# Kernel tuning notes

Hardware: AMD Instinct MI355X
Metric: run time of the kernel (lower is better)

Reference implementation:

```python
import jax, jax.numpy as jnp
import numpy as np
from jax import lax

B, C, H, W = 32, 64, 56, 56
G = 4            # num_heads*2 with num_heads=2
SMK, K = 5, 7
C2 = C // 2
HEAD_DIM = C // G
SCALE = HEAD_DIM ** -0.5


def _bias_idx(k, h, w):
    # static replica of ContMix.generate_idx + apply_rpb index construction
    rpb_size = 2 * k - 1
    idx_h = np.arange(k)
    idx_w = np.arange(k)
    idx_k = (idx_h[:, None] * rpb_size + idx_w).reshape(-1)
    rep_h = np.ones(k, np.int64); rep_h[k // 2] = h - (k - 1)
    rep_w = np.ones(k, np.int64); rep_w[k // 2] = w - (k - 1)
    bias_hw = np.repeat(idx_h, rep_h)[:, None] * rpb_size + np.repeat(idx_w, rep_w)  # (h, w)
    bias_idx = (bias_hw[..., None] + idx_k).reshape(-1, k * k)[::-1]  # torch.flip dim 0
    return jnp.asarray(bias_idx.copy())

IDX1 = _bias_idx(SMK, H, W)
IDX2 = _bias_idx(K, H, W)


def setup_inputs() -> dict:
    key = jax.random.key(0)
    ks = jax.random.split(key, 18)
    r = lambda i, sh: jax.random.normal(ks[i], sh, jnp.float32)
    return dict(
        x=r(0, (B, C, H, W)),
        lepe_w=r(1, (C, 1, K, K)) * 0.1,
        lepe_b=r(2, (C,)) * 0.1,
        lepe_bn_s=1.0 + 0.1 * r(3, (C,)),
        lepe_bn_b=0.1 * r(4, (C,)),
        wq_w=r(5, (C2, C2)) * (C2 ** -0.5),
        wq_bn_s=1.0 + 0.1 * r(6, (C2,)),
        wq_bn_b=0.1 * r(7, (C2,)),
        wk_w=r(8, (C2, C2)) * (C2 ** -0.5),
        wk_bn_s=1.0 + 0.1 * r(9, (C2,)),
        wk_bn_b=0.1 * r(10, (C2,)),
        wp_w=r(11, (SMK * SMK + K * K, 49)) * (49 ** -0.5),
        wp_b=0.1 * r(12, (SMK * SMK + K * K,)),
        rpb1=0.02 * r(13, (G, 2 * SMK - 1, 2 * SMK - 1)),
        rpb2=0.02 * r(14, (G, 2 * K - 1, 2 * K - 1)),
        dy_w=r(15, (C, C)) * (C ** -0.5),
        dy_bn_s=1.0 + 0.1 * r(16, (C,)),
        dy_bn_b=0.1 * r(17, (C,)),
    )


def _per_ch(t):
    return t[None, :, None, None]


def _contmix(x, lepe_w, lepe_b, lepe_bn_s, lepe_bn_b, wq_w, wq_bn_s, wq_bn_b,
             wk_w, wk_bn_s, wk_bn_b, wp_w, wp_b, rpb1, rpb2, dy_w, dy_bn_s, dy_bn_b):
    # lepe: deploy-mode DilatedReparamBlock = depthwise 7x7 conv (+bias), then eval BN
    lepe = lax.conv_general_dilated(x, lepe_w, (1, 1), [(K // 2, K // 2)] * 2,
                                    feature_group_count=C)
    lepe = (lepe + _per_ch(lepe_b)) * _per_ch(lepe_bn_s) + _per_ch(lepe_bn_b)

    q, kf = jnp.split(x, 2, axis=1)                         # (B, C2, H, W) each
    q = jnp.einsum('oi,bihw->bohw', wq_w, q)                # weight_query 1x1 conv
    q = (q * _per_ch(wq_bn_s) + _per_ch(wq_bn_b)) * SCALE
    # weight_key: AdaptiveAvgPool2d(7) -> 1x1 conv -> BN (H,W divisible by 7)
    kp = kf.reshape(B, C2, 7, H // 7, 7, W // 7).mean(axis=(3, 5))
    kp = jnp.einsum('oi,bihw->bohw', wk_w, kp)
    kp = kp * _per_ch(wk_bn_s) + _per_ch(wk_bn_b)

    qg = q.reshape(B, G, C2 // G, H * W)                    # b g c n
    kg = kp.reshape(B, G, C2 // G, 49)                      # b g c l
    w = jnp.einsum('bgcn,bgcl->bgnl', qg, kg)               # (B, G, HW, 49)
    # weight_proj: 1x1 conv over the 49 pooled-context channels
    w = jnp.einsum('ml,bgnl->bgnm', wp_w, w) + wp_b         # (B, G, HW, 74)
    w = w.reshape(B, G, H, W, SMK * SMK + K * K)

    attn1 = w[..., :SMK * SMK]
    attn2 = w[..., SMK * SMK:]
    attn1 = attn1 + rpb1.reshape(G, -1)[:, IDX1].reshape(1, G, H, W, SMK * SMK)
    attn2 = attn2 + rpb2.reshape(G, -1)[:, IDX2].reshape(1, G, H, W, K * K)
    attn1 = jax.nn.softmax(attn1, axis=-1)
    attn2 = jax.nn.softmax(attn2, axis=-1)

    c = C // (2 * G)                                        # value head dim = 8
    v = x.reshape(B, 2, G, c, H, W)                         # 'b (m g c) h w'

    def dyn_mix(attn, val, k):
        # unfold + einsum: content-adaptive depthwise mixing
        p = lax.conv_general_dilated_patches(
            val.reshape(B, G * c, H, W), (k, k), (1, 1), [(k // 2, k // 2)] * 2,
            dimension_numbers=('NCHW', 'OIHW', 'NCHW'))
        p = p.reshape(B, G, c, k * k, H, W)                 # channel-major patch layout
        return jnp.einsum('bgckhw,bghwk->bgchw', p, attn)

    x1 = dyn_mix(attn1, v[:, 0], SMK)
    x2 = dyn_mix(attn2, v[:, 1], K)
    out = jnp.concatenate([x1, x2], axis=1).reshape(B, C, H, W)
    out = jnp.einsum('oi,bihw->bohw', dy_w, out)            # dyconv_proj 1x1 + BN
    out = out * _per_ch(dy_bn_s) + _per_ch(dy_bn_b)
    return out + lepe


def reference(x, lepe_w, lepe_b, lepe_bn_s, lepe_bn_b, wq_w, wq_bn_s, wq_bn_b,
              wk_w, wk_bn_s, wk_bn_b, wp_w, wp_b, rpb1, rpb2, dy_w, dy_bn_s, dy_bn_b):
    return _contmix(x, lepe_w, lepe_b, lepe_bn_s, lepe_bn_b, wq_w, wq_bn_s, wq_bn_b,
                    wk_w, wk_bn_s, wk_bn_b, wp_w, wp_b, rpb1, rpb2, dy_w, dy_bn_s, dy_bn_b)
```

## Files before the change

kernel.cpp:

```cpp
#include <hip/hip_runtime.h>

#define BB 32
#define CC 64
#define HH 56
#define WW 56
#define HW 3136
#define TW 64
#define TR 12

__global__ __launch_bounds__(256) void prep_k(const float* __restrict__ x,
                                              const float* __restrict__ wk,
                                              const float* __restrict__ wks,
                                              const float* __restrict__ wkb,
                                              const float* __restrict__ wp_w,
                                              float* __restrict__ WK) {
    __shared__ float p_s[32 * 49];
    __shared__ float kg_s[8 * 49];
    const int b = blockIdx.x >> 2;
    const int g = blockIdx.x & 3;
    const int tid = threadIdx.x;
    for (int idx = tid; idx < 1568; idx += 256) {
        const int i = idx / 49, l = idx % 49;
        const int py = l / 7, px = l % 7;
        const float4* xp4 = reinterpret_cast<const float4*>(
            x + ((long)(b * CC + 32 + i)) * HW + py * 8 * WW + px * 8);
        float4 sA = make_float4(0.f, 0.f, 0.f, 0.f);
        float4 sB = make_float4(0.f, 0.f, 0.f, 0.f);
        #pragma unroll
        for (int y = 0; y < 8; ++y) {
            const float4 a = xp4[y * 14];
            const float4 c = xp4[y * 14 + 1];
            sA.x += a.x; sA.y += a.y; sA.z += a.z; sA.w += a.w;
            sB.x += c.x; sB.y += c.y; sB.z += c.z; sB.w += c.w;
        }
        p_s[idx] = (sA.x + sA.y + sA.z + sA.w + sB.x + sB.y + sB.z + sB.w) * (1.f / 64.f);
    }
    __syncthreads();
    for (int idx = tid; idx < 392; idx += 256) {
        const int o8 = idx / 49, l = idx % 49;
        const int o = g * 8 + o8;
        float acc = 0.f;
        #pragma unroll
        for (int i = 0; i < 32; ++i) acc = fmaf(wk[o * 32 + i], p_s[i * 49 + l], acc);
        kg_s[idx] = acc * wks[o] + wkb[o];
    }
    __syncthreads();
    for (int idx = tid; idx < 640; idx += 256) {
        const int c = idx / 80, slot = idx % 80;
        float acc = 0.f;
        int m = -1;
        if (slot < 28) { if (slot < 25) m = slot; }
        else           { if (slot < 77) m = 25 + (slot - 28); }
        if (m >= 0) {
            const float* kp = kg_s + c * 49;
            #pragma unroll
            for (int l = 0; l < 49; ++l) acc = fmaf(wp_w[m * 49 + l], kp[l], acc);
        }
        const long base = (long)blockIdx.x * 640;
        if (slot < 28) WK[base + c * 28 + slot] = acc;
        else           WK[base + 224 + c * 52 + (slot - 28)] = acc;
    }
}

__global__ __launch_bounds__(256) void attnmix_k(const float* __restrict__ x,
                                                 const float* __restrict__ WK,
                                                 const float* __restrict__ wq_w,
                                                 const float* __restrict__ wq_s,
                                                 const float* __restrict__ wq_bb,
                                                 const float* __restrict__ wp_b,
                                                 const float* __restrict__ rpb1,
                                                 const float* __restrict__ rpb2,
                                                 const float* __restrict__ lw,
                                                 const float* __restrict__ lb,
                                                 const float* __restrict__ ls,
                                                 const float* __restrict__ lbb,
                                                 float* __restrict__ mix,
                                                 float* __restrict__ out) {
    __shared__ float tile[8 * TR * TW];
    __shared__ float WK1_s[8 * 28];
    __shared__ float WK2_s[8 * 52];
    __shared__ float wqT_s[32 * 8];
    __shared__ float wpb1_s[25];
    __shared__ float wpb2_s[49];
    __shared__ float rpb1_s[81];
    __shared__ float rpb2_s[169];
    __shared__ float wqbn_s[16];
    __shared__ float lw_s[16 * 49];
    __shared__ float lbn_s[48];
    const int tid = threadIdx.x;
    const int bg = blockIdx.y;
    const int g = bg & 3, b = bg >> 2;

    {
        const float* wkp = WK + (long)bg * 640;
        for (int i = tid; i < 224; i += 256) WK1_s[i] = wkp[i];
        for (int i = tid; i < 416; i += 256) WK2_s[i] = wkp[224 + i];
    }
    {
        const int i = tid >> 3, c = tid & 7;
        wqT_s[tid] = wq_w[(g * 8 + c) * 32 + i];
    }
    if (tid < 25) wpb1_s[tid] = wp_b[tid];
    if (tid >= 32 && tid < 81) wpb2_s[tid - 32] = wp_b[25 + tid - 32];
    if (tid < 81) rpb1_s[tid] = rpb1[g * 81 + tid];
    if (tid < 169) rpb2_s[tid] = rpb2[g * 169 + tid];
    if (tid >= 192 && tid < 200) wqbn_s[tid - 192] = wq_s[g * 8 + tid - 192];
    if (tid >= 200 && tid < 208) wqbn_s[8 + tid - 200] = wq_bb[g * 8 + tid - 200];
    for (int i = tid; i < 784; i += 256) {
        const int ch = i / 49, k = i % 49;
        const int c = (ch < 8) ? (g * 8 + ch) : (32 + g * 8 + ch - 8);
        lw_s[i] = lw[c * 49 + k];
    }
    if (tid < 16) {
        const int c = (tid < 8) ? (g * 8 + tid) : (32 + g * 8 + tid - 8);
        lbn_s[tid] = lb[c]; lbn_s[16 + tid] = ls[c]; lbn_s[32 + tid] = lbb[c];
    }

    const int N0 = blockIdx.x << 8;
    const int ph0 = N0 / WW;
    const int r0 = ph0 - 3;

    {
        const float* xc = x + ((long)b * CC + g * 8) * HW;
        #pragma unroll
        for (int ch = 0; ch < 8; ++ch)
            for (int k = tid; k < TR * TW; k += 256) {
                const int row = k >> 6, lxx = k & 63;
                const int gy = r0 + row, gx = lxx - 3;
                float v = 0.f;
                if ((unsigned)gy < HH && (unsigned)gx < WW) v = xc[ch * HW + gy * WW + gx];
                tile[ch * (TR * TW) + k] = v;
            }
    }
    __syncthreads();

    const int n = N0 + tid;
    const bool valid = n < HW;
    const int nc = valid ? n : HW - 1;
    const int ph = nc / WW, pw = nc % WW;
    const int yr = HH - 1 - ph, xr = WW - 1 - pw;
    const int lrow = ph - r0;
    const int tb0 = (lrow - 3) * TW + pw;

    const float* xb = x + (long)b * CC * HW + nc;

    float q8[8];
    #pragma unroll
    for (int c = 0; c < 8; ++c) q8[c] = 0.f;
    for (int i = 0; i < 32; ++i) {
        const float xv = xb[i * HW];
        #pragma unroll
        for (int c = 0; c < 8; ++c) q8[c] = fmaf(wqT_s[i * 8 + c], xv, q8[c]);
    }
    #pragma unroll
    for (int c = 0; c < 8; ++c)
        q8[c] = (q8[c] * wqbn_s[c] + wqbn_s[8 + c]) * 0.25f;

    __builtin_amdgcn_sched_barrier(0);

    {
        float w1[25];
        #pragma unroll
        for (int m = 0; m < 25; ++m) w1[m] = wpb1_s[m];
        #pragma unroll
        for (int c = 0; c < 8; ++c) {
            const float qv = q8[c];
            #pragma unroll
            for (int m = 0; m < 25; ++m) w1[m] = fmaf(qv, WK1_s[c * 28 + m], w1[m]);
        }
        const int rh5 = yr < 2 ? yr : (yr > 53 ? yr - 51 : 2);
        const int rw5 = xr < 2 ? xr : (xr > 53 ? xr - 51 : 2);
        #pragma unroll
        for (int i = 0; i < 5; ++i)
            #pragma unroll
            for (int j = 0; j < 5; ++j)
                w1[i * 5 + j] += rpb1_s[(rh5 + i) * 9 + (rw5 + j)];
        float mx = -1e30f;
        #pragma unroll
        for (int m = 0; m < 25; ++m) mx = fmaxf(mx, w1[m]);
        float sm = 0.f;
        #pragma unroll
        for (int m = 0; m < 25; ++m) { w1[m] = __expf(w1[m] - mx); sm += w1[m]; }
        const float r = 1.f / sm;
        #pragma unroll
        for (int m = 0; m < 25; ++m) w1[m] *= r;

        float* m0 = mix + ((long)b * CC + g * 8) * HW + nc;
        float* o0 = out + ((long)b * CC + g * 8) * HW + nc;
        #pragma unroll
        for (int ch = 0; ch < 8; ++ch) {
            const float* t = tile + ch * (TR * TW) + tb0;
            const float* lwc = lw_s + ch * 49;
            float a = 0.f, la = 0.f;
            #pragma unroll
            for (int i = 0; i < 7; ++i)
                #pragma unroll
                for (int j = 0; j < 7; ++j) {
                    const float v = t[i * TW + j];
                    la = fmaf(lwc[i * 7 + j], v, la);
                    if (i >= 1 && i <= 5 && j >= 1 && j <= 5)
                        a = fmaf(w1[(i - 1) * 5 + (j - 1)], v, a);
                }
            if (valid) {
                m0[ch * HW] = a;
                o0[ch * HW] = (la + lbn_s[ch]) * lbn_s[16 + ch] + lbn_s[32 + ch];
            }
        }
    }

    __syncthreads();
    {
        const float* xc = x + ((long)b * CC + 32 + g * 8) * HW;
        #pragma unroll
        for (int ch = 0; ch < 8; ++ch)
            for (int k = tid; k < TR * TW; k += 256) {
                const int row = k >> 6, lxx = k & 63;
                const int gy = r0 + row, gx = lxx - 3;
                float v = 0.f;
                if ((unsigned)gy < HH && (unsigned)gx < WW) v = xc[ch * HW + gy * WW + gx];
                tile[ch * (TR * TW) + k] = v;
            }
    }
    __syncthreads();

    {
        float w2[49];
        #pragma unroll
        for (int m = 0; m < 49; ++m) w2[m] = wpb2_s[m];
        #pragma unroll
        for (int c = 0; c < 8; ++c) {
            const float qv = q8[c];
            #pragma unroll
            for (int m = 0; m < 49; ++m) w2[m] = fmaf(qv, WK2_s[c * 52 + m], w2[m]);
        }
        const int rh7 = yr < 3 ? yr : (yr > 52 ? yr - 49 : 3);
        const int rw7 = xr < 3 ? xr : (xr > 52 ? xr - 49 : 3);
        #pragma unroll
        for (int i = 0; i < 7; ++i)
            #pragma unroll
            for (int j = 0; j < 7; ++j)
                w2[i * 7 + j] += rpb2_s[(rh7 + i) * 13 + (rw7 + j)];
        float mx = -1e30f;
        #pragma unroll
        for (int m = 0; m < 49; ++m) mx = fmaxf(mx, w2[m]);
        float sm = 0.f;
        #pragma unroll
        for (int m = 0; m < 49; ++m) { w2[m] = __expf(w2[m] - mx); sm += w2[m]; }
        const float r = 1.f / sm;
        #pragma unroll
        for (int m = 0; m < 49; ++m) w2[m] *= r;

        float* m1 = mix + ((long)b * CC + 32 + g * 8) * HW + nc;
        float* o1 = out + ((long)b * CC + 32 + g * 8) * HW + nc;
        #pragma unroll
        for (int ch = 0; ch < 8; ++ch) {
            const float* t = tile + ch * (TR * TW) + tb0;
            const float* lwc = lw_s + (8 + ch) * 49;
            float a = 0.f, la = 0.f;
            #pragma unroll
            for (int i = 0; i < 7; ++i)
                #pragma unroll
                for (int j = 0; j < 7; ++j) {
                    const float v = t[i * TW + j];
                    la = fmaf(lwc[i * 7 + j], v, la);
                    a = fmaf(w2[i * 7 + j], v, a);
                }
            if (valid) {
                m1[ch * HW] = a;
                o1[ch * HW] = (la + lbn_s[8 + ch]) * lbn_s[16 + 8 + ch] + lbn_s[32 + 8 + ch];
            }
        }
    }
}

__global__ __launch_bounds__(256) void final_k(const float* __restrict__ mix,
                                               const float* __restrict__ dy_w,
                                               const float* __restrict__ s,
                                               const float* __restrict__ bb,
                                               float* __restrict__ out) {
    __shared__ float w_s[64 * 64];
    const int tid = threadIdx.x;
    const int b = blockIdx.y;
    for (int i = tid; i < 4096; i += 256) w_s[(i & 63) * 64 + (i >> 6)] = dy_w[i];
    __syncthreads();
    const int oo = (tid >> 5) * 8;
    const int p4 = blockIdx.x * 32 + (tid & 31);
    if (p4 >= 784) return;
    const float* mp = mix + (long)b * CC * HW + p4 * 4;
    float4 acc[8];
    #pragma unroll
    for (int o = 0; o < 8; ++o) acc[o] = make_float4(0.f, 0.f, 0.f, 0.f);
    for (int i = 0; i < 64; ++i) {
        const float4 mv = *reinterpret_cast<const float4*>(mp + (long)i * HW);
        const float* wr = w_s + i * 64 + oo;
        #pragma unroll
        for (int o = 0; o < 8; ++o) {
            const float wv = wr[o];
            acc[o].x = fmaf(wv, mv.x, acc[o].x);
            acc[o].y = fmaf(wv, mv.y, acc[o].y);
            acc[o].z = fmaf(wv, mv.z, acc[o].z);
            acc[o].w = fmaf(wv, mv.w, acc[o].w);
        }
    }
    float* op = out + (long)b * CC * HW + p4 * 4;
    #pragma unroll
    for (int o = 0; o < 8; ++o) {
        const float sc = s[oo + o], bc = bb[oo + o];
        float4* dst = reinterpret_cast<float4*>(op + (long)(oo + o) * HW);
        float4 prev = *dst;
        prev.x = fmaf(acc[o].x, sc, bc) + prev.x;
        prev.y = fmaf(acc[o].y, sc, bc) + prev.y;
        prev.z = fmaf(acc[o].z, sc, bc) + prev.z;
        prev.w = fmaf(acc[o].w, sc, bc) + prev.w;
        *dst = prev;
    }
}

extern "C" void kernel_launch(void* const* d_in, const int* in_sizes, int n_in,
                              void* d_out, int out_size, void* d_ws, size_t ws_size,
                              hipStream_t stream) {
    const float* x       = (const float*)d_in[0];
    const float* lepe_w  = (const float*)d_in[1];
    const float* lepe_b  = (const float*)d_in[2];
    const float* lepe_s  = (const float*)d_in[3];
    const float* lepe_bb = (const float*)d_in[4];
    const float* wq_w    = (const float*)d_in[5];
    const float* wq_s    = (const float*)d_in[6];
    const float* wq_bb   = (const float*)d_in[7];
    const float* wk_w    = (const float*)d_in[8];
    const float* wk_s    = (const float*)d_in[9];
    const float* wk_bb   = (const float*)d_in[10];
    const float* wp_w    = (const float*)d_in[11];
    const float* wp_b    = (const float*)d_in[12];
    const float* rpb1    = (const float*)d_in[13];
    const float* rpb2    = (const float*)d_in[14];
    const float* dy_w    = (const float*)d_in[15];
    const float* dy_s    = (const float*)d_in[16];
    const float* dy_bb   = (const float*)d_in[17];
    float* out = (float*)d_out;

    float* ws     = (float*)d_ws;
    float* WK_ws  = ws;
    float* mix_ws = WK_ws + 128 * 640;

    const int nTiles = (HW + 255) / 256;

    prep_k<<<dim3(BB * 4), 256, 0, stream>>>(x, wk_w, wk_s, wk_bb, wp_w, WK_ws);
    attnmix_k<<<dim3(nTiles, BB * 4), 256, 0, stream>>>(x, WK_ws, wq_w, wq_s, wq_bb,
                                                        wp_b, rpb1, rpb2,
                                                        lepe_w, lepe_b, lepe_s, lepe_bb,
                                                        mix_ws, out);
    final_k<<<dim3(25, BB), 256, 0, stream>>>(mix_ws, dy_w, dy_s, dy_bb, out);
}
```

Before: 243.5 us.

## Split pooling kernel, interleave channels in tile, read weights from global

```diff
diff --git a/kernel.cpp b/kernel.cpp
--- a/kernel.cpp
+++ b/kernel.cpp
@@ -7,8 +7,31 @@
 #define HW 3136
 #define TW 64
 #define TR 12
-
-__global__ __launch_bounds__(256) void prep_k(const float* __restrict__ x,
+#define CS 12
+
+__global__ __launch_bounds__(256) void pool_k(const float* __restrict__ x,
+                                              float* __restrict__ pool) {
+    const int idx = blockIdx.x * 256 + threadIdx.x;
+    if (idx >= BB * 32 * 49) return;
+    const int l = idx % 49;
+    const int bi = idx / 49;
+    const int i = bi % 32, b = bi / 32;
+    const int py = l / 7, px = l % 7;
+    const float4* xp4 = reinterpret_cast<const float4*>(
+        x + ((long)(b * CC + 32 + i)) * HW + py * 8 * WW + px * 8);
+    float4 sA = make_float4(0.f, 0.f, 0.f, 0.f);
+    float4 sB = make_float4(0.f, 0.f, 0.f, 0.f);
+    #pragma unroll
+    for (int y = 0; y < 8; ++y) {
+        const float4 a = xp4[y * 14];
+        const float4 c = xp4[y * 14 + 1];
+        sA.x += a.x; sA.y += a.y; sA.z += a.z; sA.w += a.w;
+        sB.x += c.x; sB.y += c.y; sB.z += c.z; sB.w += c.w;
+    }
+    pool[idx] = (sA.x + sA.y + sA.z + sA.w + sB.x + sB.y + sB.z + sB.w) * (1.f / 64.f);
+}
+
+__global__ __launch_bounds__(256) void wkwp_k(const float* __restrict__ pool,
                                               const float* __restrict__ wk,
                                               const float* __restrict__ wks,
                                               const float* __restrict__ wkb,
@@ -19,22 +42,7 @@
     const int b = blockIdx.x >> 2;
     const int g = blockIdx.x & 3;
     const int tid = threadIdx.x;
-    for (int idx = tid; idx < 1568; idx += 256) {
-        const int i = idx / 49, l = idx % 49;
-        const int py = l / 7, px = l % 7;
-        const float4* xp4 = reinterpret_cast<const float4*>(
-            x + ((long)(b * CC + 32 + i)) * HW + py * 8 * WW + px * 8);
-        float4 sA = make_float4(0.f, 0.f, 0.f, 0.f);
-        float4 sB = make_float4(0.f, 0.f, 0.f, 0.f);
-        #pragma unroll
-        for (int y = 0; y < 8; ++y) {
-            const float4 a = xp4[y * 14];
-            const float4 c = xp4[y * 14 + 1];
-            sA.x += a.x; sA.y += a.y; sA.z += a.z; sA.w += a.w;
-            sB.x += c.x; sB.y += c.y; sB.z += c.z; sB.w += c.w;
-        }
-        p_s[idx] = (sA.x + sA.y + sA.z + sA.w + sB.x + sB.y + sB.z + sB.w) * (1.f / 64.f);
-    }
+    for (int idx = tid; idx < 1568; idx += 256) p_s[idx] = pool[b * 1568 + idx];
     __syncthreads();
     for (int idx = tid; idx < 392; idx += 256) {
         const int o8 = idx / 49, l = idx % 49;
@@ -76,45 +84,20 @@
                                                  const float* __restrict__ lbb,
                                                  float* __restrict__ mix,
                                                  float* __restrict__ out) {
-    __shared__ float tile[8 * TR * TW];
-    __shared__ float WK1_s[8 * 28];
-    __shared__ float WK2_s[8 * 52];
-    __shared__ float wqT_s[32 * 8];
-    __shared__ float wpb1_s[25];
-    __shared__ float wpb2_s[49];
+    __shared__ float tile[TR * TW * CS];
     __shared__ float rpb1_s[81];
     __shared__ float rpb2_s[169];
-    __shared__ float wqbn_s[16];
-    __shared__ float lw_s[16 * 49];
-    __shared__ float lbn_s[48];
     const int tid = threadIdx.x;
     const int bg = blockIdx.y;
     const int g = bg & 3, b = bg >> 2;
-
-    {
-        const float* wkp = WK + (long)bg * 640;
-        for (int i = tid; i < 224; i += 256) WK1_s[i] = wkp[i];
-        for (int i = tid; i < 416; i += 256) WK2_s[i] = wkp[224 + i];
-    }
-    {
-        const int i = tid >> 3, c = tid & 7;
-        wqT_s[tid] = wq_w[(g * 8 + c) * 32 + i];
-    }
-    if (tid < 25) wpb1_s[tid] = wp_b[tid];
-    if (tid >= 32 && tid < 81) wpb2_s[tid - 32] = wp_b[25 + tid - 32];
     if (tid < 81) rpb1_s[tid] = rpb1[g * 81 + tid];
     if (tid < 169) rpb2_s[tid] = rpb2[g * 169 + tid];
-    if (tid >= 192 && tid < 200) wqbn_s[tid - 192] = wq_s[g * 8 + tid - 192];
-    if (tid >= 200 && tid < 208) wqbn_s[8 + tid - 200] = wq_bb[g * 8 + tid - 200];
-    for (int i = tid; i < 784; i += 256) {
-        const int ch = i / 49, k = i % 49;
-        const int c = (ch < 8) ? (g * 8 + ch) : (32 + g * 8 + ch - 8);
-        lw_s[i] = lw[c * 49 + k];
-    }
-    if (tid < 16) {
-        const int c = (tid < 8) ? (g * 8 + tid) : (32 + g * 8 + tid - 8);
-        lbn_s[tid] = lb[c]; lbn_s[16 + tid] = ls[c]; lbn_s[32 + tid] = lbb[c];
-    }
+
+    const float* WK1 = WK + (long)bg * 640;
+    const float* WK2 = WK1 + 224;
+    const float* wqp = wq_w + g * 8 * 32;
+    const float* lw0 = lw + (g * 8) * 49;
+    const float* lw1 = lw + (32 + g * 8) * 49;
 
     const int N0 = blockIdx.x << 8;
     const int ph0 = N0 / WW;
@@ -123,14 +106,17 @@
     {
         const float* xc = x + ((long)b * CC + g * 8) * HW;
         #pragma unroll
-        for (int ch = 0; ch < 8; ++ch)
-            for (int k = tid; k < TR * TW; k += 256) {
-                const int row = k >> 6, lxx = k & 63;
-                const int gy = r0 + row, gx = lxx - 3;
+        for (int ch = 0; ch < 8; ++ch) {
+            #pragma unroll
+            for (int it = 0; it < 3; ++it) {
+                const int k2 = tid + it * 256;
+                const int row = k2 >> 6, col = k2 & 63;
+                const int gy = r0 + row, gx = col - 3;
                 float v = 0.f;
                 if ((unsigned)gy < HH && (unsigned)gx < WW) v = xc[ch * HW + gy * WW + gx];
-                tile[ch * (TR * TW) + k] = v;
-            }
+                tile[k2 * CS + ch] = v;
+            }
+        }
     }
     __syncthreads();
 
@@ -140,7 +126,6 @@
     const int ph = nc / WW, pw = nc % WW;
     const int yr = HH - 1 - ph, xr = WW - 1 - pw;
     const int lrow = ph - r0;
-    const int tb0 = (lrow - 3) * TW + pw;
 
     const float* xb = x + (long)b * CC * HW + nc;
 
@@ -150,23 +135,23 @@
     for (int i = 0; i < 32; ++i) {
         const float xv = xb[i * HW];
         #pragma unroll
-        for (int c = 0; c < 8; ++c) q8[c] = fmaf(wqT_s[i * 8 + c], xv, q8[c]);
+        for (int c = 0; c < 8; ++c) q8[c] = fmaf(wqp[c * 32 + i], xv, q8[c]);
     }
     #pragma unroll
     for (int c = 0; c < 8; ++c)
-        q8[c] = (q8[c] * wqbn_s[c] + wqbn_s[8 + c]) * 0.25f;
+        q8[c] = (q8[c] * wq_s[g * 8 + c] + wq_bb[g * 8 + c]) * 0.25f;
 
     __builtin_amdgcn_sched_barrier(0);
 
     {
         float w1[25];
         #pragma unroll
-        for (int m = 0; m < 25; ++m) w1[m] = wpb1_s[m];
+        for (int m = 0; m < 25; ++m) w1[m] = wp_b[m];
         #pragma unroll
         for (int c = 0; c < 8; ++c) {
             const float qv = q8[c];
             #pragma unroll
-            for (int m = 0; m < 25; ++m) w1[m] = fmaf(qv, WK1_s[c * 28 + m], w1[m]);
+            for (int m = 0; m < 25; ++m) w1[m] = fmaf(qv, WK1[c * 28 + m], w1[m]);
         }
         const int rh5 = yr < 2 ? yr : (yr > 53 ? yr - 51 : 2);
         const int rw5 = xr < 2 ? xr : (xr > 53 ? xr - 51 : 2);
@@ -185,25 +170,35 @@
         #pragma unroll
         for (int m = 0; m < 25; ++m) w1[m] *= r;
 
+        float acc[8], lacc[8];
+        #pragma unroll
+        for (int ch = 0; ch < 8; ++ch) { acc[ch] = 0.f; lacc[ch] = 0.f; }
+        #pragma unroll
+        for (int i = 0; i < 7; ++i) {
+            #pragma unroll
+            for (int j = 0; j < 7; ++j) {
+                const float* t = &tile[((lrow - 3 + i) * TW + pw + j) * CS];
+                const float4 va = *reinterpret_cast<const float4*>(t);
+                const float4 vb = *reinterpret_cast<const float4*>(t + 4);
+                const float v[8] = {va.x, va.y, va.z, va.w, vb.x, vb.y, vb.z, vb.w};
+                #pragma unroll
+                for (int ch = 0; ch < 8; ++ch)
+                    lacc[ch] = fmaf(lw0[ch * 49 + i * 7 + j], v[ch], lacc[ch]);
+                if (i >= 1 && i <= 5 && j >= 1 && j <= 5) {
+                    const float wv = w1[(i - 1) * 5 + (j - 1)];
+                    #pragma unroll
+                    for (int ch = 0; ch < 8; ++ch)
+                        acc[ch] = fmaf(wv, v[ch], acc[ch]);
+                }
+            }
+        }
         float* m0 = mix + ((long)b * CC + g * 8) * HW + nc;
         float* o0 = out + ((long)b * CC + g * 8) * HW + nc;
-        #pragma unroll
-        for (int ch = 0; ch < 8; ++ch) {
-            const float* t = tile + ch * (TR * TW) + tb0;
-            const float* lwc = lw_s + ch * 49;
-            float a = 0.f, la = 0.f;
-            #pragma unroll
-            for (int i = 0; i < 7; ++i)
-                #pragma unroll
-                for (int j = 0; j < 7; ++j) {
-                    const float v = t[i * TW + j];
-                    la = fmaf(lwc[i * 7 + j], v, la);
-                    if (i >= 1 && i <= 5 && j >= 1 && j <= 5)
-                        a = fmaf(w1[(i - 1) * 5 + (j - 1)], v, a);
-                }
-            if (valid) {
-                m0[ch * HW] = a;
-                o0[ch * HW] = (la + lbn_s[ch]) * lbn_s[16 + ch] + lbn_s[32 + ch];
+        if (valid) {
+            #pragma unroll
+            for (int ch = 0; ch < 8; ++ch) {
+                m0[ch * HW] = acc[ch];
+                o0[ch * HW] = (lacc[ch] + lb[g * 8 + ch]) * ls[g * 8 + ch] + lbb[g * 8 + ch];
             }
         }
     }
@@ -212,26 +207,29 @@
     {
         const float* xc = x + ((long)b * CC + 32 + g * 8) * HW;
         #pragma unroll
-        for (int ch = 0; ch < 8; ++ch)
-            for (int k = tid; k < TR * TW; k += 256) {
-                const int row = k >> 6, lxx = k & 63;
-                const int gy = r0 + row, gx = lxx - 3;
+        for (int ch = 0; ch < 8; ++ch) {
+            #pragma unroll
+            for (int it = 0; it < 3; ++it) {
+                const int k2 = tid + it * 256;
+                const int row = k2 >> 6, col = k2 & 63;
+                const int gy = r0 + row, gx = col - 3;
                 float v = 0.f;
                 if ((unsigned)gy < HH && (unsigned)gx < WW) v = xc[ch * HW + gy * WW + gx];
-                tile[ch * (TR * TW) + k] = v;
-            }
+                tile[k2 * CS + ch] = v;
+            }
+        }
     }
     __syncthreads();
 
     {
         float w2[49];
         #pragma unroll
-        for (int m = 0; m < 49; ++m) w2[m] = wpb2_s[m];
+        for (int m = 0; m < 49; ++m) w2[m] = wp_b[25 + m];
         #pragma unroll
         for (int c = 0; c < 8; ++c) {
             const float qv = q8[c];
             #pragma unroll
-            for (int m = 0; m < 49; ++m) w2[m] = fmaf(qv, WK2_s[c * 52 + m], w2[m]);
+            for (int m = 0; m < 49; ++m) w2[m] = fmaf(qv, WK2[c * 52 + m], w2[m]);
         }
         const int rh7 = yr < 3 ? yr : (yr > 52 ? yr - 49 : 3);
         const int rw7 = xr < 3 ? xr : (xr > 52 ? xr - 49 : 3);
@@ -250,24 +248,33 @@
         #pragma unroll
         for (int m = 0; m < 49; ++m) w2[m] *= r;
 
+        float acc[8], lacc[8];
+        #pragma unroll
+        for (int ch = 0; ch < 8; ++ch) { acc[ch] = 0.f; lacc[ch] = 0.f; }
+        #pragma unroll
+        for (int i = 0; i < 7; ++i) {
+            #pragma unroll
+            for (int j = 0; j < 7; ++j) {
+                const float* t = &tile[((lrow - 3 + i) * TW + pw + j) * CS];
+                const float4 va = *reinterpret_cast<const float4*>(t);
+                const float4 vb = *reinterpret_cast<const float4*>(t + 4);
+                const float v[8] = {va.x, va.y, va.z, va.w, vb.x, vb.y, vb.z, vb.w};
+                const float wv = w2[i * 7 + j];
+                #pragma unroll
+                for (int ch = 0; ch < 8; ++ch) {
+                    lacc[ch] = fmaf(lw1[ch * 49 + i * 7 + j], v[ch], lacc[ch]);
+                    acc[ch] = fmaf(wv, v[ch], acc[ch]);
+                }
+            }
+        }
         float* m1 = mix + ((long)b * CC + 32 + g * 8) * HW + nc;
         float* o1 = out + ((long)b * CC + 32 + g * 8) * HW + nc;
-        #pragma unroll
-        for (int ch = 0; ch < 8; ++ch) {
-            const float* t = tile + ch * (TR * TW) + tb0;
-            const float* lwc = lw_s + (8 + ch) * 49;
-            float a = 0.f, la = 0.f;
-            #pragma unroll
-            for (int i = 0; i < 7; ++i)
-                #pragma unroll
-                for (int j = 0; j < 7; ++j) {
-                    const float v = t[i * TW + j];
-                    la = fmaf(lwc[i * 7 + j], v, la);
-                    a = fmaf(w2[i * 7 + j], v, a);
-                }
-            if (valid) {
-                m1[ch * HW] = a;
-                o1[ch * HW] = (la + lbn_s[8 + ch]) * lbn_s[16 + 8 + ch] + lbn_s[32 + 8 + ch];
+        if (valid) {
+            #pragma unroll
+            for (int ch = 0; ch < 8; ++ch) {
+                m1[ch * HW] = acc[ch];
+                o1[ch * HW] = (lacc[ch] + lb[32 + g * 8 + ch]) * ls[32 + g * 8 + ch]
+                              + lbb[32 + g * 8 + ch];
             }
         }
     }
@@ -339,13 +346,15 @@
     const float* dy_bb   = (const float*)d_in[17];
     float* out = (float*)d_out;
 
-    float* ws     = (float*)d_ws;
-    float* WK_ws  = ws;
-    float* mix_ws = WK_ws + 128 * 640;
+    float* ws      = (float*)d_ws;
+    float* pool_ws = ws;
+    float* WK_ws   = pool_ws + 32 * 32 * 49;
+    float* mix_ws  = WK_ws + 128 * 640;
 
     const int nTiles = (HW + 255) / 256;
 
-    prep_k<<<dim3(BB * 4), 256, 0, stream>>>(x, wk_w, wk_s, wk_bb, wp_w, WK_ws);
+    pool_k<<<dim3((BB * 32 * 49 + 255) / 256), 256, 0, stream>>>(x, pool_ws);
+    wkwp_k<<<dim3(BB * 4), 256, 0, stream>>>(pool_ws, wk_w, wk_s, wk_bb, wp_w, WK_ws);
     attnmix_k<<<dim3(nTiles, BB * 4), 256, 0, stream>>>(x, WK_ws, wq_w, wq_s, wq_bb,
                                                         wp_b, rpb1, rpb2,
                                                         lepe_w, lepe_b, lepe_s, lepe_bb,
```

After: 346.5 us. +42.3%, slower.

## Split pooling into its own kernel and read stencil directly from global memory

Applied to the files above, without the earlier changes.

```diff
diff --git a/kernel.cpp b/kernel.cpp
--- a/kernel.cpp
+++ b/kernel.cpp
@@ -5,10 +5,30 @@
 #define HH 56
 #define WW 56
 #define HW 3136
-#define TW 64
-#define TR 12
-
-__global__ __launch_bounds__(256) void prep_k(const float* __restrict__ x,
+
+__global__ __launch_bounds__(256) void pool_k(const float* __restrict__ x,
+                                              float* __restrict__ pool) {
+    const int idx = blockIdx.x * 256 + threadIdx.x;
+    if (idx >= BB * 32 * 49) return;
+    const int l = idx % 49;
+    const int bi = idx / 49;
+    const int i = bi % 32, b = bi / 32;
+    const int py = l / 7, px = l % 7;
+    const float4* xp4 = reinterpret_cast<const float4*>(
+        x + ((long)(b * CC + 32 + i)) * HW + py * 8 * WW + px * 8);
+    float4 sA = make_float4(0.f, 0.f, 0.f, 0.f);
+    float4 sB = make_float4(0.f, 0.f, 0.f, 0.f);
+    #pragma unroll
+    for (int y = 0; y < 8; ++y) {
+        const float4 a = xp4[y * 14];
+        const float4 c = xp4[y * 14 + 1];
+        sA.x += a.x; sA.y += a.y; sA.z += a.z; sA.w += a.w;
+        sB.x += c.x; sB.y += c.y; sB.z += c.z; sB.w += c.w;
+    }
+    pool[idx] = (sA.x + sA.y + sA.z + sA.w + sB.x + sB.y + sB.z + sB.w) * (1.f / 64.f);
+}
+
+__global__ __launch_bounds__(256) void wkwp_k(const float* __restrict__ pool,
                                               const float* __restrict__ wk,
                                               const float* __restrict__ wks,
                                               const float* __restrict__ wkb,
@@ -19,22 +39,7 @@
     const int b = blockIdx.x >> 2;
     const int g = blockIdx.x & 3;
     const int tid = threadIdx.x;
-    for (int idx = tid; idx < 1568; idx += 256) {
-        const int i = idx / 49, l = idx % 49;
-        const int py = l / 7, px = l % 7;
-        const float4* xp4 = reinterpret_cast<const float4*>(
-            x + ((long)(b * CC + 32 + i)) * HW + py * 8 * WW + px * 8);
-        float4 sA = make_float4(0.f, 0.f, 0.f, 0.f);
-        float4 sB = make_float4(0.f, 0.f, 0.f, 0.f);
-        #pragma unroll
-        for (int y = 0; y < 8; ++y) {
-            const float4 a = xp4[y * 14];
-            const float4 c = xp4[y * 14 + 1];
-            sA.x += a.x; sA.y += a.y; sA.z += a.z; sA.w += a.w;
-            sB.x += c.x; sB.y += c.y; sB.z += c.z; sB.w += c.w;
-        }
-        p_s[idx] = (sA.x + sA.y + sA.z + sA.w + sB.x + sB.y + sB.z + sB.w) * (1.f / 64.f);
-    }
+    for (int idx = tid; idx < 1568; idx += 256) p_s[idx] = pool[b * 1568 + idx];
     __syncthreads();
     for (int idx = tid; idx < 392; idx += 256) {
         const int o8 = idx / 49, l = idx % 49;
@@ -76,7 +81,6 @@
                                                  const float* __restrict__ lbb,
                                                  float* __restrict__ mix,
                                                  float* __restrict__ out) {
-    __shared__ float tile[8 * TR * TW];
     __shared__ float WK1_s[8 * 28];
     __shared__ float WK2_s[8 * 52];
     __shared__ float wqT_s[32 * 8];
@@ -90,7 +94,6 @@
     const int tid = threadIdx.x;
     const int bg = blockIdx.y;
     const int g = bg & 3, b = bg >> 2;
-
     {
         const float* wkp = WK + (long)bg * 640;
         for (int i = tid; i < 224; i += 256) WK1_s[i] = wkp[i];
@@ -115,34 +118,14 @@
         const int c = (tid < 8) ? (g * 8 + tid) : (32 + g * 8 + tid - 8);
         lbn_s[tid] = lb[c]; lbn_s[16 + tid] = ls[c]; lbn_s[32 + tid] = lbb[c];
     }
-
-    const int N0 = blockIdx.x << 8;
-    const int ph0 = N0 / WW;
-    const int r0 = ph0 - 3;
-
-    {
-        const float* xc = x + ((long)b * CC + g * 8) * HW;
-        #pragma unroll
-        for (int ch = 0; ch < 8; ++ch)
-            for (int k = tid; k < TR * TW; k += 256) {
-                const int row = k >> 6, lxx = k & 63;
-                const int gy = r0 + row, gx = lxx - 3;
-                float v = 0.f;
-                if ((unsigned)gy < HH && (unsigned)gx < WW) v = xc[ch * HW + gy * WW + gx];
-                tile[ch * (TR * TW) + k] = v;
-            }
-    }
     __syncthreads();
-
-    const int n = N0 + tid;
-    const bool valid = n < HW;
-    const int nc = valid ? n : HW - 1;
-    const int ph = nc / WW, pw = nc % WW;
+    const int n = blockIdx.x * 256 + tid;
+    if (n >= HW) return;
+
+    const int ph = n / WW, pw = n % WW;
     const int yr = HH - 1 - ph, xr = WW - 1 - pw;
-    const int lrow = ph - r0;
-    const int tb0 = (lrow - 3) * TW + pw;
-
-    const float* xb = x + (long)b * CC * HW + nc;
+
+    const float* xb = x + (long)b * CC * HW + n;
 
     float q8[8];
     #pragma unroll
@@ -185,43 +168,44 @@
         #pragma unroll
         for (int m = 0; m < 25; ++m) w1[m] *= r;
 
-        float* m0 = mix + ((long)b * CC + g * 8) * HW + nc;
-        float* o0 = out + ((long)b * CC + g * 8) * HW + nc;
+        const float* vb = xb + (long)(g * 8) * HW;
+        float acc[8], lacc[8];
+        #pragma unroll
+        for (int ch = 0; ch < 8; ++ch) { acc[ch] = 0.f; lacc[ch] = 0.f; }
+        #pragma unroll
+        for (int i = 0; i < 7; ++i) {
+            const int y = ph + i - 3;
+            if ((unsigned)y >= HH) continue;
+            #pragma unroll
+            for (int j = 0; j < 7; ++j) {
+                const int xx = pw + j - 3;
+                if ((unsigned)xx >= WW) continue;
+                const int off = (i - 3) * WW + (j - 3);
+                if (i >= 1 && i <= 5 && j >= 1 && j <= 5) {
+                    const float wv = w1[(i - 1) * 5 + (j - 1)];
+                    #pragma unroll
+                    for (int ch = 0; ch < 8; ++ch) {
+                        const float v = vb[ch * HW + off];
+                        lacc[ch] = fmaf(lw_s[ch * 49 + i * 7 + j], v, lacc[ch]);
+                        acc[ch] = fmaf(wv, v, acc[ch]);
+                    }
+                } else {
+                    #pragma unroll
+                    for (int ch = 0; ch < 8; ++ch)
+                        lacc[ch] = fmaf(lw_s[ch * 49 + i * 7 + j], vb[ch * HW + off], lacc[ch]);
+                }
+            }
+        }
+        float* m0 = mix + ((long)b * CC + g * 8) * HW + n;
+        float* o0 = out + ((long)b * CC + g * 8) * HW + n;
         #pragma unroll
         for (int ch = 0; ch < 8; ++ch) {
-            const float* t = tile + ch * (TR * TW) + tb0;
-            const float* lwc = lw_s + ch * 49;
-            float a = 0.f, la = 0.f;
-            #pragma unroll
-            for (int i = 0; i < 7; ++i)
-                #pragma unroll
-                for (int j = 0; j < 7; ++j) {
-                    const float v = t[i * TW + j];
-                    la = fmaf(lwc[i * 7 + j], v, la);
-                    if (i >= 1 && i <= 5 && j >= 1 && j <= 5)
-                        a = fmaf(w1[(i - 1) * 5 + (j - 1)], v, a);
-                }
-            if (valid) {
-                m0[ch * HW] = a;
-                o0[ch * HW] = (la + lbn_s[ch]) * lbn_s[16 + ch] + lbn_s[32 + ch];
-            }
-        }
-    }
-
-    __syncthreads();
-    {
-        const float* xc = x + ((long)b * CC + 32 + g * 8) * HW;
-        #pragma unroll
-        for (int ch = 0; ch < 8; ++ch)
-            for (int k = tid; k < TR * TW; k += 256) {
-                const int row = k >> 6, lxx = k & 63;
-                const int gy = r0 + row, gx = lxx - 3;
-                float v = 0.f;
-                if ((unsigned)gy < HH && (unsigned)gx < WW) v = xc[ch * HW + gy * WW + gx];
-                tile[ch * (TR * TW) + k] = v;
-            }
-    }
-    __syncthreads();
+            m0[ch * HW] = acc[ch];
+            o0[ch * HW] = (lacc[ch] + lbn_s[ch]) * lbn_s[16 + ch] + lbn_s[32 + ch];
+        }
+    }
+
+    __builtin_amdgcn_sched_barrier(0);
 
     {
         float w2[49];
@@ -250,25 +234,34 @@
         #pragma unroll
         for (int m = 0; m < 49; ++m) w2[m] *= r;
 
-        float* m1 = mix + ((long)b * CC + 32 + g * 8) * HW + nc;
-        float* o1 = out + ((long)b * CC + 32 + g * 8) * HW + nc;
+        const float* vb = xb + (long)(32 + g * 8) * HW;
+        float acc[8], lacc[8];
+        #pragma unroll
+        for (int ch = 0; ch < 8; ++ch) { acc[ch] = 0.f; lacc[ch] = 0.f; }
+        #pragma unroll
+        for (int i = 0; i < 7; ++i) {
+            const int y = ph + i - 3;
+            if ((unsigned)y >= HH) continue;
+            #pragma unroll
+            for (int j = 0; j < 7; ++j) {
+                const int xx = pw + j - 3;
+                if ((unsigned)xx >= WW) continue;
+                const int off = (i - 3) * WW + (j - 3);
+                const float wv = w2[i * 7 + j];
+                #pragma unroll
+                for (int ch = 0; ch < 8; ++ch) {
+                    const float v = vb[ch * HW + off];
+                    lacc[ch] = fmaf(lw_s[(8 + ch) * 49 + i * 7 + j], v, lacc[ch]);
+                    acc[ch] = fmaf(wv, v, acc[ch]);
+                }
+            }
+        }
+        float* m1 = mix + ((long)b * CC + 32 + g * 8) * HW + n;
+        float* o1 = out + ((long)b * CC + 32 + g * 8) * HW + n;
         #pragma unroll
         for (int ch = 0; ch < 8; ++ch) {
-            const float* t = tile + ch * (TR * TW) + tb0;
-            const float* lwc = lw_s + (8 + ch) * 49;
-            float a = 0.f, la = 0.f;
-            #pragma unroll
-            for (int i = 0; i < 7; ++i)
-                #pragma unroll
-                for (int j = 0; j < 7; ++j) {
-                    const float v = t[i * TW + j];
-                    la = fmaf(lwc[i * 7 + j], v, la);
-                    a = fmaf(w2[i * 7 + j], v, a);
-                }
-            if (valid) {
-                m1[ch * HW] = a;
-                o1[ch * HW] = (la + lbn_s[8 + ch]) * lbn_s[16 + 8 + ch] + lbn_s[32 + 8 + ch];
-            }
+            m1[ch * HW] = acc[ch];
+            o1[ch * HW] = (lacc[ch] + lbn_s[8 + ch]) * lbn_s[16 + 8 + ch] + lbn_s[32 + 8 + ch];
         }
     }
 }
@@ -339,13 +332,15 @@
     const float* dy_bb   = (const float*)d_in[17];
     float* out = (float*)d_out;
 
-    float* ws     = (float*)d_ws;
-    float* WK_ws  = ws;
-    float* mix_ws = WK_ws + 128 * 640;
+    float* ws      = (float*)d_ws;
+    float* pool_ws = ws;
+    float* WK_ws   = pool_ws + 32 * 32 * 49;
+    float* mix_ws  = WK_ws + 128 * 640;
 
     const int nTiles = (HW + 255) / 256;
 
-    prep_k<<<dim3(BB * 4), 256, 0, stream>>>(x, wk_w, wk_s, wk_bb, wp_w, WK_ws);
+    pool_k<<<dim3((BB * 32 * 49 + 255) / 256), 256, 0, stream>>>(x, pool_ws);
+    wkwp_k<<<dim3(BB * 4), 256, 0, stream>>>(pool_ws, wk_w, wk_s, wk_bb, wp_w, WK_ws);
     attnmix_k<<<dim3(nTiles, BB * 4), 256, 0, stream>>>(x, WK_ws, wq_w, wq_s, wq_bb,
                                                         wp_b, rpb1, rpb2,
                                                         lepe_w, lepe_b, lepe_s, lepe_bb,
```

New measurement: 409.8 us. +68.3%, slower.
